# Kernel optimization log

Measured on AMD Instinct MI355X. Metric: run time of the kernel, lower is better.

## Reference

```python
import jax, jax.numpy as jnp
import numpy as np

MARGIN = 1.0
N, D = 8192, 256
NUM_CLASSES = 32


def setup_inputs() -> dict:
    key = jax.random.key(0)
    k1, k2 = jax.random.split(key)
    embeddings = jax.random.normal(k1, (N, D), dtype=jnp.float32)
    labels = jax.random.randint(k2, (N,), 0, NUM_CLASSES, dtype=jnp.int64)
    return {"embeddings": embeddings, "labels": labels}


def reference(embeddings, labels):
    # L2-normalize rows (F.normalize p=2 dim=1); subsequent cosine similarity
    # of unit vectors is just their dot product -> plain [N, N] matmul.
    e = embeddings / jnp.linalg.norm(embeddings, axis=1, keepdims=True)
    sim = e @ e.T  # [N, N] cosine similarity matrix

    pos_mask = (labels[:, None] == labels[None, :])  # [N, N] bool
    pos_count = jnp.sum(pos_mask)
    neg_count = pos_mask.size - pos_count

    # Fused masked-mean reductions (no boolean gather / dynamic shapes).
    pos_term = jnp.where(pos_mask, (1.0 - sim) ** 2, 0.0)
    neg_term = jnp.where(pos_mask, 0.0, jax.nn.relu(sim - MARGIN) ** 2)
    positive_loss = jnp.sum(pos_term) / pos_count
    negative_loss = jnp.sum(neg_term) / neg_count
    return positive_loss + negative_loss
```

## Files before the change

### kernel.cpp

```cpp
#include <hip/hip_runtime.h>
#include <hip/hip_bf16.h>
#include <stdint.h>

#define N_ROWS 8192
#define DIM 256
#define NUM_CLASSES 32
#define PC 384
#define TPC 6
#define NBLK3 (NUM_CLASSES * TPC)

typedef __attribute__((ext_vector_type(4))) float f32x4;
typedef __attribute__((ext_vector_type(8))) short bf16x8;

static __device__ inline unsigned short f2bf(float f) {
  union { float f; unsigned u; } v; v.f = f;
  unsigned r = v.u + 0x7FFFu + ((v.u >> 16) & 1u);
  return (unsigned short)(r >> 16);
}

static __device__ inline void async_copy16(const void* g, void* l) {
  __builtin_amdgcn_global_load_lds(
      (const __attribute__((address_space(1))) unsigned int*)g,
      (__attribute__((address_space(3))) unsigned int*)l, 16, 0, 0);
}

__global__ __launch_bounds__(256)
void norm_prep_kernel(const float* __restrict__ emb,
                      const int* __restrict__ labels,
                      unsigned short* __restrict__ en,
                      unsigned short* __restrict__ rowlist,
                      int* __restrict__ cnt,
                      float* __restrict__ acc,
                      int* __restrict__ counter) {
  const int t = threadIdx.x;
  if (blockIdx.x < 2048) {
    const int row = blockIdx.x * 4 + (t >> 6);
    const int lane = t & 63;
    const float4 v = reinterpret_cast<const float4*>(emb + (size_t)row * DIM)[lane];
    float s = v.x * v.x + v.y * v.y + v.z * v.z + v.w * v.w;
    #pragma unroll
    for (int o = 32; o; o >>= 1) s += __shfl_xor(s, o);
    const float inv = 1.0f / sqrtf(s);
    ushort4 o4;
    o4.x = f2bf(v.x * inv);
    o4.y = f2bf(v.y * inv);
    o4.z = f2bf(v.z * inv);
    o4.w = f2bf(v.w * inv);
    reinterpret_cast<ushort4*>(en + (size_t)row * DIM)[lane] = o4;
    return;
  }

  const int c = blockIdx.x - 2048;
  __shared__ int rk;
  if (t == 0) rk = 0;
  __syncthreads();
  for (int i = t; i < N_ROWS; i += 256) {
    if (labels[i] == c) {
      const int r = atomicAdd(&rk, 1);
      if (r < PC) rowlist[c * PC + r] = (unsigned short)i;
    }
  }
  __syncthreads();
  const int nc = rk;
  if (t == 0) cnt[c] = nc;
  for (int i = nc + t; i < PC; i += 256) rowlist[c * PC + i] = (unsigned short)N_ROWS;
  if (c == 0) {
    if (t < 128) ((int*)(en + (size_t)N_ROWS * DIM))[t] = 0;
    if (t == 0) { acc[0] = 0.f; acc[1] = 0.f; counter[0] = 0; }
  }
}

__global__ __launch_bounds__(256)
void class_sim_kernel(const unsigned short* __restrict__ en,
                      const unsigned short* __restrict__ rowlist,
                      const int* __restrict__ cnt,
                      float* __restrict__ acc,
                      int* __restrict__ counter,
                      float* __restrict__ out) {
  const int b = blockIdx.x;
  const int c = b / TPC, q = b - c * TPC;
  const int ti = (q < 3) ? 0 : (q < 5) ? 1 : 2;
  const int tj = (q < 3) ? q : (q < 5) ? (q - 2) : 2;
  const int t = threadIdx.x;
  const int nc = cnt[c];
  const bool active = (ti * 128 < nc) && (tj * 128 < nc);

  float s1 = 0.f, s2 = 0.f;

  if (active) {
    __shared__ __align__(16) short lA[2][128 * 64];
    __shared__ __align__(16) short lB[2][128 * 64];
    __shared__ float red[8];

    const int lane = t & 63;
    const int wid = t >> 6;
    const int r15 = lane & 15;
    const int wm = (wid >> 1) * 64;
    const int wn = (wid & 1) * 64;

    int rA[4], rB[4];
    #pragma unroll
    for (int it = 0; it < 4; ++it) {
      rA[it] = rowlist[c * PC + ti * 128 + it * 32 + (t >> 3)];
      rB[it] = rowlist[c * PC + tj * 128 + it * 32 + (t >> 3)];
    }
    const int cb = (((t & 7) ^ ((t >> 3) & 7)) << 4);

    auto stage = [&](int buf, int kt) {
      const int kb = kt * 128;
      #pragma unroll
      for (int it = 0; it < 4; ++it) {
        const int x = (it * 256 + t) * 16;
        async_copy16((const char*)en + (size_t)rA[it] * 512 + kb + cb,
                     (char*)&lA[buf][0] + x);
        async_copy16((const char*)en + (size_t)rB[it] * 512 + kb + cb,
                     (char*)&lB[buf][0] + x);
      }
    };

    f32x4 accf[4][4];
    #pragma unroll
    for (int i = 0; i < 4; ++i)
      #pragma unroll
      for (int j = 0; j < 4; ++j) accf[i][j] = (f32x4){0.f, 0.f, 0.f, 0.f};

    stage(0, 0);
    __syncthreads();

    int cur = 0;
    #pragma unroll
    for (int kt = 0; kt < 4; ++kt) {
      if (kt < 3) stage(cur ^ 1, kt + 1);

      #pragma unroll
      for (int kk = 0; kk < 2; ++kk) {
        const int cbase = kk * 64 + ((lane >> 4) << 4);
        bf16x8 af[4], bf[4];
        #pragma unroll
        for (int mi = 0; mi < 4; ++mi) {
          const int row = wm + mi * 16 + r15;
          const int off = row * 128 + (cbase ^ ((row & 7) << 4));
          af[mi] = *(const bf16x8*)((const char*)&lA[cur][0] + off);
        }
        #pragma unroll
        for (int ni = 0; ni < 4; ++ni) {
          const int row = wn + ni * 16 + r15;
          const int off = row * 128 + (cbase ^ ((row & 7) << 4));
          bf[ni] = *(const bf16x8*)((const char*)&lB[cur][0] + off);
        }
        #pragma unroll
        for (int mi = 0; mi < 4; ++mi)
          #pragma unroll
          for (int ni = 0; ni < 4; ++ni)
            accf[mi][ni] = __builtin_amdgcn_mfma_f32_16x16x32_bf16(
                af[mi], bf[ni], accf[mi][ni], 0, 0, 0);
      }

      if (kt < 3) { __syncthreads(); cur ^= 1; }
    }

    #pragma unroll
    for (int mi = 0; mi < 4; ++mi)
      #pragma unroll
      for (int ni = 0; ni < 4; ++ni)
        #pragma unroll
        for (int j = 0; j < 4; ++j) {
          const float s = accf[mi][ni][j];
          s1 += s;
          s2 += s * s;
        }
    if (ti != tj) { s1 *= 2.f; s2 *= 2.f; }

    #pragma unroll
    for (int o = 32; o; o >>= 1) { s1 += __shfl_down(s1, o); s2 += __shfl_down(s2, o); }
    if (lane == 0) { red[wid * 2] = s1; red[wid * 2 + 1] = s2; }
    __syncthreads();
    if (t == 0) {
      s1 = red[0] + red[2] + red[4] + red[6];
      s2 = red[1] + red[3] + red[5] + red[7];
    }
  }

  if (t == 0) {
    if (active) {
      atomicAdd(&acc[0], s1);
      atomicAdd(&acc[1], s2);
    }
    __threadfence();
    const int prev = atomicAdd(counter, 1);
    if (prev == NBLK3 - 1) {
      __threadfence();
      const float ts1 = atomicAdd(&acc[0], 0.f);
      const float ts2 = atomicAdd(&acc[1], 0.f);
      float P = 0.f;
      for (int cc = 0; cc < NUM_CLASSES; ++cc) {
        const float n = (float)cnt[cc];
        P += n * n;
      }
      out[0] = (P - 2.f * ts1 + ts2) / P;
    }
  }
}

extern "C" void kernel_launch(void* const* d_in, const int* in_sizes, int n_in,
                              void* d_out, int out_size, void* d_ws, size_t ws_size,
                              hipStream_t stream) {
  const float* emb = (const float*)d_in[0];
  const int* labels = (const int*)d_in[1];
  float* out = (float*)d_out;

  unsigned short* en = (unsigned short*)d_ws;
  char* p = (char*)d_ws + (size_t)(N_ROWS + 1) * DIM * 2;
  unsigned short* rowlist = (unsigned short*)p;
  p += NUM_CLASSES * PC * 2;
  int* cnt = (int*)p;
  p += NUM_CLASSES * 4;
  float* acc = (float*)p;
  p += 4 * 4;
  int* counter = (int*)p;

  norm_prep_kernel<<<2048 + NUM_CLASSES, 256, 0, stream>>>(emb, labels, en, rowlist,
                                                           cnt, acc, counter);
  class_sim_kernel<<<NBLK3, 256, 0, stream>>>(en, rowlist, cnt, acc, counter, out);
}
```

Before: 28.79 us.

## Fuse normalization and class bucketing into single per-class similarity kernel

Merges the normalize/prep kernel and the class-similarity kernel into one launch. Each block scans the labels itself to build its class row list in shared memory, loads the raw fp32 rows, converts them to bf16 directly into swizzled LDS tiles holding the full K dimension, and applies the inverse norms after the MFMA as scaling factors. This removes the bf16 workspace round-trip and the second kernel launch, at the cost of each of the 192 blocks scanning all labels redundantly and losing the async double-buffered loads. A memset now zeroes the accumulators, and P is accumulated through an atomic.

```diff
diff --git a/kernel.cpp b/kernel.cpp
--- a/kernel.cpp
+++ b/kernel.cpp
@@ -7,7 +7,7 @@
 #define NUM_CLASSES 32
 #define PC 384
 #define TPC 6
-#define NBLK3 (NUM_CLASSES * TPC)
+#define NBLK (NUM_CLASSES * TPC)
 
 typedef __attribute__((ext_vector_type(4))) float f32x4;
 typedef __attribute__((ext_vector_type(8))) short bf16x8;
@@ -18,105 +18,74 @@
   return (unsigned short)(r >> 16);
 }
 
-static __device__ inline void async_copy16(const void* g, void* l) {
-  __builtin_amdgcn_global_load_lds(
-      (const __attribute__((address_space(1))) unsigned int*)g,
-      (__attribute__((address_space(3))) unsigned int*)l, 16, 0, 0);
-}
+__global__ __launch_bounds__(256)
+void fused_loss_kernel(const float* __restrict__ emb,
+                       const int* __restrict__ labels,
+                       float* __restrict__ acc,
+                       int* __restrict__ counter,
+                       float* __restrict__ out) {
+  const int b = blockIdx.x;
+  const int c = b / TPC, q = b - c * TPC;
+  const int ti = (q < 3) ? 0 : (q < 5) ? 1 : 2;
+  const int tj = (q < 3) ? q : (q < 5) ? (q - 2) : 2;
+  const int t = threadIdx.x;
+  const int lane = t & 63;
+  const int wid = t >> 6;
+  const int r15 = lane & 15;
 
-__global__ __launch_bounds__(256)
-void norm_prep_kernel(const float* __restrict__ emb,
-                      const int* __restrict__ labels,
-                      unsigned short* __restrict__ en,
-                      unsigned short* __restrict__ rowlist,
-                      int* __restrict__ cnt,
-                      float* __restrict__ acc,
-                      int* __restrict__ counter) {
-  const int t = threadIdx.x;
-  if (blockIdx.x < 2048) {
-    const int row = blockIdx.x * 4 + (t >> 6);
-    const int lane = t & 63;
-    const float4 v = reinterpret_cast<const float4*>(emb + (size_t)row * DIM)[lane];
-    float s = v.x * v.x + v.y * v.y + v.z * v.z + v.w * v.w;
-    #pragma unroll
-    for (int o = 32; o; o >>= 1) s += __shfl_xor(s, o);
-    const float inv = 1.0f / sqrtf(s);
-    ushort4 o4;
-    o4.x = f2bf(v.x * inv);
-    o4.y = f2bf(v.y * inv);
-    o4.z = f2bf(v.z * inv);
-    o4.w = f2bf(v.w * inv);
-    reinterpret_cast<ushort4*>(en + (size_t)row * DIM)[lane] = o4;
-    return;
-  }
+  __shared__ __align__(16) short lA[128 * 256];
+  __shared__ __align__(16) short lB[128 * 256];
+  __shared__ unsigned short rows_c[PC];
+  __shared__ float invs[256];
+  __shared__ float red[8];
+  __shared__ int rk;
 
-  const int c = blockIdx.x - 2048;
-  __shared__ int rk;
+  for (int i = t; i < PC; i += 256) rows_c[i] = 0xFFFF;
   if (t == 0) rk = 0;
   __syncthreads();
   for (int i = t; i < N_ROWS; i += 256) {
     if (labels[i] == c) {
       const int r = atomicAdd(&rk, 1);
-      if (r < PC) rowlist[c * PC + r] = (unsigned short)i;
+      if (r < PC) rows_c[r] = (unsigned short)i;
     }
   }
   __syncthreads();
-  const int nc = rk;
-  if (t == 0) cnt[c] = nc;
-  for (int i = nc + t; i < PC; i += 256) rowlist[c * PC + i] = (unsigned short)N_ROWS;
-  if (c == 0) {
-    if (t < 128) ((int*)(en + (size_t)N_ROWS * DIM))[t] = 0;
-    if (t == 0) { acc[0] = 0.f; acc[1] = 0.f; counter[0] = 0; }
-  }
-}
-
-__global__ __launch_bounds__(256)
-void class_sim_kernel(const unsigned short* __restrict__ en,
-                      const unsigned short* __restrict__ rowlist,
-                      const int* __restrict__ cnt,
-                      float* __restrict__ acc,
-                      int* __restrict__ counter,
-                      float* __restrict__ out) {
-  const int b = blockIdx.x;
-  const int c = b / TPC, q = b - c * TPC;
-  const int ti = (q < 3) ? 0 : (q < 5) ? 1 : 2;
-  const int tj = (q < 3) ? q : (q < 5) ? (q - 2) : 2;
-  const int t = threadIdx.x;
-  const int nc = cnt[c];
+  const int nc = (rk < PC) ? rk : PC;
   const bool active = (ti * 128 < nc) && (tj * 128 < nc);
 
-  float s1 = 0.f, s2 = 0.f;
+  float s1t = 0.f, s2t = 0.f;
 
   if (active) {
-    __shared__ __align__(16) short lA[2][128 * 64];
-    __shared__ __align__(16) short lB[2][128 * 64];
-    __shared__ float red[8];
+    const int slot = (t < 128) ? (ti * 128 + t) : (tj * 128 + (t - 128));
+    const int idx = rows_c[slot];
+    short* tile = (t < 128) ? lA : lB;
+    const int row = t & 127;
+    const int swz = (row & 7) << 4;
+    char* const rbase = (char*)tile + row * 512;
+    float sum = 0.f;
+    if (idx != 0xFFFF) {
+      const float4* rp = (const float4*)(emb + (size_t)idx * DIM);
+      #pragma unroll 8
+      for (int j = 0; j < 64; ++j) {
+        const float4 v = rp[j];
+        sum += v.x * v.x + v.y * v.y + v.z * v.z + v.w * v.w;
+        ushort4 o;
+        o.x = f2bf(v.x); o.y = f2bf(v.y); o.z = f2bf(v.z); o.w = f2bf(v.w);
+        *(ushort4*)(rbase + ((j * 8) ^ swz)) = o;
+      }
+      invs[t] = rsqrtf(sum);
+    } else {
+      const ushort4 z = {0, 0, 0, 0};
+      #pragma unroll 8
+      for (int j = 0; j < 64; ++j) *(ushort4*)(rbase + ((j * 8) ^ swz)) = z;
+      invs[t] = 0.f;
+    }
+    __syncthreads();
 
-    const int lane = t & 63;
-    const int wid = t >> 6;
-    const int r15 = lane & 15;
     const int wm = (wid >> 1) * 64;
     const int wn = (wid & 1) * 64;
-
-    int rA[4], rB[4];
-    #pragma unroll
-    for (int it = 0; it < 4; ++it) {
-      rA[it] = rowlist[c * PC + ti * 128 + it * 32 + (t >> 3)];
-      rB[it] = rowlist[c * PC + tj * 128 + it * 32 + (t >> 3)];
-    }
-    const int cb = (((t & 7) ^ ((t >> 3) & 7)) << 4);
-
-    auto stage = [&](int buf, int kt) {
-      const int kb = kt * 128;
-      #pragma unroll
-      for (int it = 0; it < 4; ++it) {
-        const int x = (it * 256 + t) * 16;
-        async_copy16((const char*)en + (size_t)rA[it] * 512 + kb + cb,
-                     (char*)&lA[buf][0] + x);
-        async_copy16((const char*)en + (size_t)rB[it] * 512 + kb + cb,
-                     (char*)&lB[buf][0] + x);
-      }
-    };
+    const int kq = (lane >> 4) << 4;
+    const int sw = (r15 & 7) << 4;
 
     f32x4 accf[4][4];
     #pragma unroll
@@ -124,48 +93,45 @@
       #pragma unroll
       for (int j = 0; j < 4; ++j) accf[i][j] = (f32x4){0.f, 0.f, 0.f, 0.f};
 
-    stage(0, 0);
-    __syncthreads();
-
-    int cur = 0;
     #pragma unroll
-    for (int kt = 0; kt < 4; ++kt) {
-      if (kt < 3) stage(cur ^ 1, kt + 1);
-
+    for (int kc = 0; kc < 8; ++kc) {
+      const int cbase = kc * 64 + kq;
+      bf16x8 af[4], bf[4];
       #pragma unroll
-      for (int kk = 0; kk < 2; ++kk) {
-        const int cbase = kk * 64 + ((lane >> 4) << 4);
-        bf16x8 af[4], bf[4];
+      for (int mi = 0; mi < 4; ++mi) {
+        const int r = wm + mi * 16 + r15;
+        af[mi] = *(const bf16x8*)((const char*)lA + r * 512 + (cbase ^ sw));
+      }
+      #pragma unroll
+      for (int ni = 0; ni < 4; ++ni) {
+        const int r = wn + ni * 16 + r15;
+        bf[ni] = *(const bf16x8*)((const char*)lB + r * 512 + (cbase ^ sw));
+      }
+      #pragma unroll
+      for (int mi = 0; mi < 4; ++mi)
         #pragma unroll
-        for (int mi = 0; mi < 4; ++mi) {
-          const int row = wm + mi * 16 + r15;
-          const int off = row * 128 + (cbase ^ ((row & 7) << 4));
-          af[mi] = *(const bf16x8*)((const char*)&lA[cur][0] + off);
-        }
-        #pragma unroll
-        for (int ni = 0; ni < 4; ++ni) {
-          const int row = wn + ni * 16 + r15;
-          const int off = row * 128 + (cbase ^ ((row & 7) << 4));
-          bf[ni] = *(const bf16x8*)((const char*)&lB[cur][0] + off);
-        }
-        #pragma unroll
-        for (int mi = 0; mi < 4; ++mi)
-          #pragma unroll
-          for (int ni = 0; ni < 4; ++ni)
-            accf[mi][ni] = __builtin_amdgcn_mfma_f32_16x16x32_bf16(
-                af[mi], bf[ni], accf[mi][ni], 0, 0, 0);
-      }
-
-      if (kt < 3) { __syncthreads(); cur ^= 1; }
+        for (int ni = 0; ni < 4; ++ni)
+          accf[mi][ni] = __builtin_amdgcn_mfma_f32_16x16x32_bf16(
+              af[mi], bf[ni], accf[mi][ni], 0, 0, 0);
     }
 
+    const int r4 = (lane >> 4) << 2;
+    float ia[16], ib[4];
+    #pragma unroll
+    for (int mi = 0; mi < 4; ++mi)
+      #pragma unroll
+      for (int j = 0; j < 4; ++j) ia[mi * 4 + j] = invs[wm + mi * 16 + r4 + j];
+    #pragma unroll
+    for (int ni = 0; ni < 4; ++ni) ib[ni] = invs[128 + wn + ni * 16 + r15];
+
+    float s1 = 0.f, s2 = 0.f;
     #pragma unroll
     for (int mi = 0; mi < 4; ++mi)
       #pragma unroll
       for (int ni = 0; ni < 4; ++ni)
         #pragma unroll
         for (int j = 0; j < 4; ++j) {
-          const float s = accf[mi][ni][j];
+          const float s = accf[mi][ni][j] * ia[mi * 4 + j] * ib[ni];
           s1 += s;
           s2 += s * s;
         }
@@ -176,28 +142,21 @@
     if (lane == 0) { red[wid * 2] = s1; red[wid * 2 + 1] = s2; }
     __syncthreads();
     if (t == 0) {
-      s1 = red[0] + red[2] + red[4] + red[6];
-      s2 = red[1] + red[3] + red[5] + red[7];
+      s1t = red[0] + red[2] + red[4] + red[6];
+      s2t = red[1] + red[3] + red[5] + red[7];
     }
   }
 
   if (t == 0) {
-    if (active) {
-      atomicAdd(&acc[0], s1);
-      atomicAdd(&acc[1], s2);
-    }
-    __threadfence();
+    if (q == 0) { const float n = (float)nc; atomicAdd(&acc[2], n * n); }
+    if (active) { atomicAdd(&acc[0], s1t); atomicAdd(&acc[1], s2t); }
+    asm volatile("s_waitcnt vmcnt(0)" ::: "memory");
     const int prev = atomicAdd(counter, 1);
-    if (prev == NBLK3 - 1) {
-      __threadfence();
-      const float ts1 = atomicAdd(&acc[0], 0.f);
-      const float ts2 = atomicAdd(&acc[1], 0.f);
-      float P = 0.f;
-      for (int cc = 0; cc < NUM_CLASSES; ++cc) {
-        const float n = (float)cnt[cc];
-        P += n * n;
-      }
-      out[0] = (P - 2.f * ts1 + ts2) / P;
+    if (prev == NBLK - 1) {
+      const float S1 = atomicAdd(&acc[0], 0.f);
+      const float S2 = atomicAdd(&acc[1], 0.f);
+      const float P  = atomicAdd(&acc[2], 0.f);
+      out[0] = (P - 2.f * S1 + S2) / P;
     }
   }
 }
@@ -209,17 +168,9 @@
   const int* labels = (const int*)d_in[1];
   float* out = (float*)d_out;
 
-  unsigned short* en = (unsigned short*)d_ws;
-  char* p = (char*)d_ws + (size_t)(N_ROWS + 1) * DIM * 2;
-  unsigned short* rowlist = (unsigned short*)p;
-  p += NUM_CLASSES * PC * 2;
-  int* cnt = (int*)p;
-  p += NUM_CLASSES * 4;
-  float* acc = (float*)p;
-  p += 4 * 4;
-  int* counter = (int*)p;
+  float* acc = (float*)d_ws;
+  int* counter = (int*)((char*)d_ws + 12);
 
-  norm_prep_kernel<<<2048 + NUM_CLASSES, 256, 0, stream>>>(emb, labels, en, rowlist,
-                                                           cnt, acc, counter);
-  class_sim_kernel<<<NBLK3, 256, 0, stream>>>(en, rowlist, cnt, acc, counter, out);
+  hipMemsetAsync(d_ws, 0, 16, stream);
+  fused_loss_kernel<<<NBLK, 256, 0, stream>>>(emb, labels, acc, counter, out);
 }
```

Result: slower. 31.78 us (+10.4%).
